# Kernel tuning notes

Measured on AMD Instinct MI355X. Metric: run time of the kernel, lower is better.

## Reference

```python
import jax, jax.numpy as jnp
import numpy as np

N, E, D, H = 50000, 800000, 128, 4
EPS = 1e-5


def setup_inputs() -> dict:
    key = jax.random.key(0)
    ks = jax.random.split(key, 12)
    s_in = 1.0 / np.sqrt(D)
    s_att = 1.0 / np.sqrt(D)
    inp = {
        "x": jax.random.normal(ks[0], (N, D), dtype=jnp.float32),
        "edge_index": jax.random.randint(ks[1], (2, E), 0, N, dtype=jnp.int32),
        # conv1 params: W [D, H*D], att_src/att_dst [H, D], bias [D]
        "W1": jax.random.normal(ks[2], (D, H * D), dtype=jnp.float32) * s_in,
        "as1": jax.random.normal(ks[3], (H, D), dtype=jnp.float32) * s_att,
        "ad1": jax.random.normal(ks[4], (H, D), dtype=jnp.float32) * s_att,
        "b1": jnp.zeros((D,), dtype=jnp.float32),
        "g1": jnp.ones((D,), dtype=jnp.float32),
        "be1": jnp.zeros((D,), dtype=jnp.float32),
        # conv2 params
        "W2": jax.random.normal(ks[5], (D, H * D), dtype=jnp.float32) * s_in,
        "as2": jax.random.normal(ks[6], (H, D), dtype=jnp.float32) * s_att,
        "ad2": jax.random.normal(ks[7], (H, D), dtype=jnp.float32) * s_att,
        "b2": jnp.zeros((D,), dtype=jnp.float32),
        "g2": jnp.ones((D,), dtype=jnp.float32),
        "be2": jnp.zeros((D,), dtype=jnp.float32),
    }
    return inp


def _gat_conv(x, src, dst, W, att_src, att_dst, bias):
    # project: [N, H, C]
    h = (x @ W).reshape(N, H, D)
    a_src = jnp.einsum("nhc,hc->nh", h, att_src)  # [N, H]
    a_dst = jnp.einsum("nhc,hc->nh", h, att_dst)  # [N, H]
    # attention logits per edge, softmax over incoming edges of each dst
    logits = jax.nn.leaky_relu(a_src[src] + a_dst[dst], negative_slope=0.2)  # [Etot, H]
    lmax = jax.ops.segment_max(logits, dst, num_segments=N)  # [N, H]
    p = jnp.exp(logits - lmax[dst])
    denom = jax.ops.segment_sum(p, dst, num_segments=N)  # [N, H]
    alpha = p / denom[dst]  # self-loops guarantee denom > 0
    # weighted scatter-add aggregation
    msg = h[src] * alpha[:, :, None]  # [Etot, H, C]
    out = jax.ops.segment_sum(msg, dst, num_segments=N)  # [N, H, C]
    return out.mean(axis=1) + bias  # concat=False: mean over heads


def _batchnorm_relu(x, gamma, beta):
    mu = x.mean(axis=0)
    var = x.var(axis=0)  # biased, as torch uses for normalization
    xn = (x - mu) * jax.lax.rsqrt(var + EPS)
    return jax.nn.relu(xn * gamma + beta)


def reference(x, edge_index, W1, as1, ad1, b1, g1, be1, W2, as2, ad2, b2, g2, be2):
    # add self loops (GATConv default add_self_loops=True)
    loop = jnp.arange(N, dtype=edge_index.dtype)
    src = jnp.concatenate([edge_index[0], loop])
    dst = jnp.concatenate([edge_index[1], loop])
    x = _batchnorm_relu(_gat_conv(x, src, dst, W1, as1, ad1, b1), g1, be1)
    x = _batchnorm_relu(_gat_conv(x, src, dst, W2, as2, ad2, b2), g2, be2)
    return x
```

## Files before the change

kernel.cpp:

```cpp
#include <hip/hip_runtime.h>
#include <hip/hip_bf16.h>
#include <hip/hip_fp16.h>
#include <math.h>

#define NN 50000
#define NP 50048
#define NE 800000
#define ET (NE + NN)
#define DF 128
#define NH 4
#define HD 512
#define BN_EPS 1e-5f

typedef __hip_bfloat16 bf16;
typedef __attribute__((ext_vector_type(8))) short bf16x8;
typedef __attribute__((ext_vector_type(4))) float f32x4;
typedef __attribute__((ext_vector_type(2))) float f32x2;

__global__ __launch_bounds__(256) void cvt_x_bf16(const float* __restrict__ in, bf16* __restrict__ out) {
    int i = blockIdx.x * 256 + threadIdx.x;
    if (i >= NN * DF / 4) return;
    float4 v = reinterpret_cast<const float4*>(in)[i];
    union { bf16 b[4]; short4 s; } u;
    u.b[0] = __float2bfloat16(v.x); u.b[1] = __float2bfloat16(v.y);
    u.b[2] = __float2bfloat16(v.z); u.b[3] = __float2bfloat16(v.w);
    reinterpret_cast<short4*>(out)[i] = u.s;
}

__global__ __launch_bounds__(256) void make_wsd(const float* __restrict__ W1, const float* __restrict__ as1,
                                                const float* __restrict__ ad1,
                                                const float* __restrict__ W2, const float* __restrict__ as2,
                                                const float* __restrict__ ad2,
                                                float* __restrict__ wsd) {
    int t = blockIdx.x * 256 + threadIdx.x;
    if (t >= 2048) return;
    int layer = t >> 10;
    int o = (t >> 7) & 7;
    int d = t & 127;
    int h = o & 3;
    const float* W  = layer ? W2 : W1;
    const float* av = layer ? (o < 4 ? as2 : ad2) : (o < 4 ? as1 : ad1);
    const float* wrow = W + d * HD + h * DF;
    const float* arow = av + h * DF;
    float sum = 0.f;
    for (int c = 0; c < DF; ++c) sum += wrow[c] * arow[c];
    wsd[layer * 1024 + o * DF + d] = sum;
}

__global__ __launch_bounds__(256) void cvt_bt2(const float* __restrict__ W1, const float* __restrict__ W2,
                                               bf16* __restrict__ B1, bf16* __restrict__ B2) {
    int i = blockIdx.x * 256 + threadIdx.x;
    if (i >= 2 * DF * HD) return;
    int layer = i >> 16;
    int ii = i & 65535;
    int c = ii >> 9, k = ii & 511;
    int h = k >> 7, d = k & 127;
    const float* W = layer ? W2 : W1;
    bf16* B = layer ? B2 : B1;
    B[ii] = __float2bfloat16(0.25f * W[d * HD + h * DF + c]);
}

__global__ __launch_bounds__(256) void xscore(const bf16* __restrict__ X,
                                              const float* __restrict__ wsd,
                                              float* __restrict__ a_src,
                                              float* __restrict__ a_dst,
                                              float* __restrict__ stats) {
    if (blockIdx.x == 0 && threadIdx.x < 64)
        reinterpret_cast<float4*>(stats)[threadIdx.x] = make_float4(0.f, 0.f, 0.f, 0.f);
    __shared__ float w[8][DF];
    reinterpret_cast<float4*>(&w[0][0])[threadIdx.x] = reinterpret_cast<const float4*>(wsd)[threadIdx.x];
    __syncthreads();
    const int n = blockIdx.x * 4 + (threadIdx.x >> 6);
    const int l = threadIdx.x & 63;
    unsigned xv = reinterpret_cast<const unsigned*>(X)[n * 64 + l];
    float x0 = __uint_as_float(xv << 16);
    float x1 = __uint_as_float(xv & 0xffff0000u);
    float v[8];
    #pragma unroll
    for (int o = 0; o < 8; ++o)
        v[o] = x0 * w[o][2 * l] + x1 * w[o][2 * l + 1];
    #pragma unroll
    for (int off = 1; off < 64; off <<= 1) {
        #pragma unroll
        for (int o = 0; o < 8; ++o) v[o] += __shfl_xor(v[o], off);
    }
    if (l == 0) {
        reinterpret_cast<float4*>(a_src)[n] = make_float4(v[0], v[1], v[2], v[3]);
        reinterpret_cast<float4*>(a_dst)[n] = make_float4(v[4], v[5], v[6], v[7]);
    }
}

__global__ __launch_bounds__(256) void count_rank(const int* __restrict__ ei, int* __restrict__ counts,
                                                  int* __restrict__ rank) {
    int e = (blockIdx.x * 256 + threadIdx.x) * 2;
    if (e >= ET) return;
    int d0, d1;
    if (e + 1 < NE) {
        int2 dd = *reinterpret_cast<const int2*>(ei + NE + e);
        d0 = dd.x; d1 = dd.y;
    } else {
        d0 = (e < NE) ? ei[NE + e] : (e - NE);
        d1 = (e + 1 < NE) ? ei[NE + e + 1] : (e + 1 - NE);
    }
    rank[e]     = atomicAdd(&counts[d0 << 4], 1);
    rank[e + 1] = atomicAdd(&counts[d1 << 4], 1);
}

__global__ __launch_bounds__(256) void scan1(const int* __restrict__ counts, int* __restrict__ bsum) {
    __shared__ int sd[256];
    int i = blockIdx.x * 256 + threadIdx.x;
    sd[threadIdx.x] = (i < NN) ? counts[i << 4] : 0;
    __syncthreads();
    for (int s = 128; s > 0; s >>= 1) {
        if (threadIdx.x < s) sd[threadIdx.x] += sd[threadIdx.x + s];
        __syncthreads();
    }
    if (threadIdx.x == 0) bsum[blockIdx.x] = sd[0];
}

__global__ __launch_bounds__(256) void scan2(int* __restrict__ bsum, int nb) {
    __shared__ int sd[256];
    int i = threadIdx.x;
    int v = (i < nb) ? bsum[i] : 0;
    sd[i] = v;
    __syncthreads();
    for (int s = 1; s < 256; s <<= 1) {
        int t = sd[i];
        int u = (i >= s) ? sd[i - s] : 0;
        __syncthreads();
        sd[i] = t + u;
        __syncthreads();
    }
    if (i < nb) bsum[i] = sd[i] - v;
}

__global__ __launch_bounds__(256) void scan3(const int* __restrict__ counts, const int* __restrict__ bsum,
                                             int* __restrict__ row_ptr) {
    __shared__ int sd[256];
    int i = blockIdx.x * 256 + threadIdx.x;
    int v = (i < NN) ? counts[i << 4] : 0;
    sd[threadIdx.x] = v;
    __syncthreads();
    for (int s = 1; s < 256; s <<= 1) {
        int t = sd[threadIdx.x];
        int u = (threadIdx.x >= s) ? sd[threadIdx.x - s] : 0;
        __syncthreads();
        sd[threadIdx.x] = t + u;
        __syncthreads();
    }
    int excl = sd[threadIdx.x] - v + bsum[blockIdx.x];
    if (i < NN) row_ptr[i] = excl;
    if (i == 0) row_ptr[NN] = ET;
}

__global__ __launch_bounds__(256) void fill_scatter(const int* __restrict__ ei, const int* __restrict__ rank,
                                                    const int* __restrict__ row_ptr, int* __restrict__ col) {
    int e = (blockIdx.x * 256 + threadIdx.x) * 2;
    if (e >= ET) return;
    int s0, d0, s1, d1;
    if (e + 1 < NE) {
        int2 ss = *reinterpret_cast<const int2*>(ei + e);
        int2 dd = *reinterpret_cast<const int2*>(ei + NE + e);
        s0 = ss.x; s1 = ss.y; d0 = dd.x; d1 = dd.y;
    } else {
        if (e < NE) { s0 = ei[e]; d0 = ei[NE + e]; } else { s0 = d0 = e - NE; }
        if (e + 1 < NE) { s1 = ei[e + 1]; d1 = ei[NE + e + 1]; } else { s1 = d1 = e + 1 - NE; }
    }
    int2 rk = *reinterpret_cast<const int2*>(rank + e);
    col[row_ptr[d0] + rk.x] = s0;
    col[row_ptr[d1] + rk.y] = s1;
}

#define EDGEF(xu, pa) {                                                              \
    f32x2 xv;                                                                        \
    xv.x = __uint_as_float((xu) << 16);                                              \
    xv.y = __uint_as_float((xu) & 0xffff0000u);                                      \
    acc2[0] += (pa).x * xv;                                                          \
    acc2[1] += (pa).y * xv;                                                          \
    acc2[2] += (pa).z * xv;                                                          \
    acc2[3] += (pa).w * xv; }

#define EDGE(xu, r) {                                                                \
    f32x2 xv;                                                                        \
    xv.x = __uint_as_float((xu) << 16);                                              \
    xv.y = __uint_as_float((xu) & 0xffff0000u);                                      \
    float2 f01 = __half22float2(*reinterpret_cast<const __half2*>(&(r).x));          \
    float2 f23 = __half22float2(*reinterpret_cast<const __half2*>(&(r).y));          \
    acc2[0] += f01.x * xv;                                                           \
    acc2[1] += f01.y * xv;                                                           \
    acc2[2] += f23.x * xv;                                                           \
    acc2[3] += f23.y * xv; }

__global__ __launch_bounds__(256) void agg_fused(const bf16* __restrict__ X,
                                                 const float* __restrict__ a_src,
                                                 const float* __restrict__ a_dst,
                                                 const int* __restrict__ row_ptr,
                                                 const int* __restrict__ col,
                                                 uint4* __restrict__ rec,
                                                 bf16* __restrict__ aggX) {
    __shared__ __align__(16) float4 lalpha[4][64];
    __shared__ unsigned lcol[4][64];
    const int w = threadIdx.x >> 6;
    const int n = blockIdx.x * 4 + w;
    const int l = threadIdx.x & 63;
    const unsigned l4 = (unsigned)l << 2;
    const int start = row_ptr[n], end = row_ptr[n + 1];
    const int deg = end - start;
    const float4 ad4 = reinterpret_cast<const float4*>(a_dst)[n];
    const float4* __restrict__ as4 = reinterpret_cast<const float4*>(a_src);
    const char* __restrict__ Xb = reinterpret_cast<const char*>(X);
    f32x2 acc2[4] = {};
    if (deg <= 64) {
        const int j = start + l;
        int cj = 0;
        float lv[4] = {-1e30f, -1e30f, -1e30f, -1e30f};
        if (j < end) {
            cj = col[j];
            float4 a = as4[cj];
            lv[0] = a.x + ad4.x; lv[1] = a.y + ad4.y; lv[2] = a.z + ad4.z; lv[3] = a.w + ad4.w;
            #pragma unroll
            for (int h = 0; h < 4; ++h) lv[h] = lv[h] > 0.f ? lv[h] : 0.2f * lv[h];
        }
        float m[4], p[4], s[4];
        #pragma unroll
        for (int h = 0; h < 4; ++h) m[h] = lv[h];
        #pragma unroll
        for (int off = 1; off < 64; off <<= 1) {
            #pragma unroll
            for (int h = 0; h < 4; ++h) m[h] = fmaxf(m[h], __shfl_xor(m[h], off));
        }
        #pragma unroll
        for (int h = 0; h < 4; ++h) { p[h] = (j < end) ? __expf(lv[h] - m[h]) : 0.f; s[h] = p[h]; }
        #pragma unroll
        for (int off = 1; off < 64; off <<= 1) {
            #pragma unroll
            for (int h = 0; h < 4; ++h) s[h] += __shfl_xor(s[h], off);
        }
        lalpha[w][l] = make_float4(p[0] / s[0], p[1] / s[1], p[2] / s[2], p[3] / s[3]);
        lcol[w][l] = (unsigned)cj << 8;
        __builtin_amdgcn_wave_barrier();
        for (int i = 0; i < deg; i += 4) {
            float4 pa0 = lalpha[w][i],     pa1 = lalpha[w][i + 1];
            float4 pa2 = lalpha[w][i + 2], pa3 = lalpha[w][i + 3];
            unsigned o0 = lcol[w][i] | l4,     o1 = lcol[w][i + 1] | l4;
            unsigned o2 = lcol[w][i + 2] | l4, o3 = lcol[w][i + 3] | l4;
            unsigned x0 = *reinterpret_cast<const unsigned*>(Xb + o0);
            unsigned x1 = *reinterpret_cast<const unsigned*>(Xb + o1);
            unsigned x2 = *reinterpret_cast<const unsigned*>(Xb + o2);
            unsigned x3 = *reinterpret_cast<const unsigned*>(Xb + o3);
            EDGEF(x0, pa0) EDGEF(x1, pa1) EDGEF(x2, pa2) EDGEF(x3, pa3)
        }
    } else {
        float m[4] = {-1e30f, -1e30f, -1e30f, -1e30f}, s[4] = {0.f, 0.f, 0.f, 0.f};
        for (int base = start; base < end; base += 64) {
            const int j = base + l;
            float lv[4] = {-1e30f, -1e30f, -1e30f, -1e30f};
            if (j < end) {
                float4 a = as4[col[j]];
                lv[0] = a.x + ad4.x; lv[1] = a.y + ad4.y; lv[2] = a.z + ad4.z; lv[3] = a.w + ad4.w;
                #pragma unroll
                for (int h = 0; h < 4; ++h) lv[h] = lv[h] > 0.f ? lv[h] : 0.2f * lv[h];
            }
            float cm[4], cp[4];
            #pragma unroll
            for (int h = 0; h < 4; ++h) cm[h] = lv[h];
            #pragma unroll
            for (int off = 1; off < 64; off <<= 1) {
                #pragma unroll
                for (int h = 0; h < 4; ++h) cm[h] = fmaxf(cm[h], __shfl_xor(cm[h], off));
            }
            #pragma unroll
            for (int h = 0; h < 4; ++h) {
                float nm = fmaxf(m[h], cm[h]);
                cp[h] = (j < end) ? __expf(lv[h] - nm) : 0.f;
                s[h] *= __expf(m[h] - nm);
                m[h] = nm;
            }
            #pragma unroll
            for (int off = 1; off < 64; off <<= 1) {
                #pragma unroll
                for (int h = 0; h < 4; ++h) cp[h] += __shfl_xor(cp[h], off);
            }
            #pragma unroll
            for (int h = 0; h < 4; ++h) s[h] += cp[h];
        }
        for (int base = start; base < end; base += 64) {
            const int j = base + l;
            if (j < end) {
                int cj = col[j];
                float4 a = as4[cj];
                float v0 = a.x + ad4.x, v1 = a.y + ad4.y, v2 = a.z + ad4.z, v3 = a.w + ad4.w;
                v0 = v0 > 0.f ? v0 : 0.2f * v0; v1 = v1 > 0.f ? v1 : 0.2f * v1;
                v2 = v2 > 0.f ? v2 : 0.2f * v2; v3 = v3 > 0.f ? v3 : 0.2f * v3;
                __half2 a01 = __floats2half2_rn(__expf(v0 - m[0]) / s[0], __expf(v1 - m[1]) / s[1]);
                __half2 a23 = __floats2half2_rn(__expf(v2 - m[2]) / s[2], __expf(v3 - m[3]) / s[3]);
                uint4 r;
                r.x = *reinterpret_cast<unsigned*>(&a01);
                r.y = *reinterpret_cast<unsigned*>(&a23);
                r.z = (unsigned)cj;
                r.w = 0;
                rec[j] = r;
            }
        }
        __threadfence_block();
        const unsigned* __restrict__ X4 = reinterpret_cast<const unsigned*>(X);
        int j = start;
        for (; j + 4 <= end; j += 4) {
            uint4 r0 = rec[j], r1 = rec[j + 1], r2 = rec[j + 2], r3 = rec[j + 3];
            unsigned x0 = X4[(size_t)r0.z * 64 + l];
            unsigned x1 = X4[(size_t)r1.z * 64 + l];
            unsigned x2 = X4[(size_t)r2.z * 64 + l];
            unsigned x3 = X4[(size_t)r3.z * 64 + l];
            EDGE(x0, r0) EDGE(x1, r1) EDGE(x2, r2) EDGE(x3, r3)
        }
        for (; j < end; ++j) {
            uint4 r0 = rec[j];
            unsigned x0 = X4[(size_t)r0.z * 64 + l];
            EDGE(x0, r0)
        }
    }
    unsigned* outp = reinterpret_cast<unsigned*>(aggX) + (size_t)n * 256;
    #pragma unroll
    for (int h = 0; h < 4; ++h) {
        union { bf16 b; unsigned short u; } plo, phi;
        plo.b = __float2bfloat16(acc2[h].x);
        phi.b = __float2bfloat16(acc2[h].y);
        outp[h * 64 + l] = (unsigned)plo.u | ((unsigned)phi.u << 16);
    }
}

__global__ __launch_bounds__(256) void gemm_out(const bf16* __restrict__ A,
                                                const bf16* __restrict__ Bt,
                                                const float* __restrict__ bias,
                                                bf16* __restrict__ outb,
                                                float* __restrict__ stats, int M) {
    __shared__ __align__(16) char Bs[65536];
    __shared__ float ssum[128], ssq[128];
    const int tid = threadIdx.x;
    if (tid < 128) { ssum[tid] = 0.f; ssq[tid] = 0.f; }
    const int m0 = blockIdx.x * 64;
    const char* Ab = (const char*)A + (size_t)m0 * 1024;
    const char* Bb = (const char*)Bt;
    auto stageB = [&](int ph) {
        #pragma unroll
        for (int i = 0; i < 16; ++i) {
            int d = (tid + i * 256) * 16;
            int c = d >> 9;
            int kb = d & 511;
            int src = c * 1024 + ph * 512 + (kb ^ ((c & 7) << 4));
            __builtin_amdgcn_global_load_lds(
                (const __attribute__((address_space(1))) void*)(Bb + src),
                (__attribute__((address_space(3))) void*)(Bs + d), 16, 0, 0);
        }
    };
    const int lane = tid & 63;
    const int wave = tid >> 6;
    const int wm = (wave & 1) * 32;
    const int wnb = (wave >> 1) * 64;
    const int lr = lane & 15;
    const int lkb = (lane >> 4) * 16;
    f32x4 acc[2][4] = {};
    const char* arow0 = Ab + (size_t)(wm + lr) * 1024 + lkb;
    const char* arow1 = Ab + (size_t)(wm + 16 + lr) * 1024 + lkb;
    stageB(0);
    #pragma unroll
    for (int ph = 0; ph < 2; ++ph) {
        __syncthreads();
        #pragma unroll 4
        for (int kk = 0; kk < 8; ++kk) {
            int kg = ph * 512 + kk * 64;
            bf16x8 a0 = *(const bf16x8*)(arow0 + kg);
            bf16x8 a1 = *(const bf16x8*)(arow1 + kg);
            int kb = kk * 64 + lkb;
            #pragma unroll
            for (int nf = 0; nf < 4; ++nf) {
                int c = wnb + nf * 16 + lr;
                bf16x8 b = *(const bf16x8*)(Bs + c * 512 + (kb ^ ((c & 7) << 4)));
                acc[0][nf] = __builtin_amdgcn_mfma_f32_16x16x32_bf16(a0, b, acc[0][nf], 0, 0, 0);
                acc[1][nf] = __builtin_amdgcn_mfma_f32_16x16x32_bf16(a1, b, acc[1][nf], 0, 0, 0);
            }
        }
        if (ph == 0) {
            __syncthreads();
            stageB(1);
        }
    }
    const int orow = (lane >> 4) * 4;
    float bcol[4];
    #pragma unroll
    for (int nf = 0; nf < 4; ++nf) bcol[nf] = bias[wnb + nf * 16 + lr];
    #pragma unroll
    for (int nf = 0; nf < 4; ++nf) {
        float cs = 0.f, cq = 0.f;
        int c = wnb + nf * 16 + lr;
        #pragma unroll
        for (int mi = 0; mi < 2; ++mi) {
            #pragma unroll
            for (int r = 0; r < 4; ++r) {
                int gr = m0 + wm + mi * 16 + orow + r;
                if (gr < M) {
                    float v = acc[mi][nf][r] + bcol[nf];
                    outb[(size_t)gr * DF + c] = __float2bfloat16(v);
                    cs += v; cq += v * v;
                }
            }
        }
        atomicAdd(&ssum[c], cs);
        atomicAdd(&ssq[c], cq);
    }
    __syncthreads();
    if (tid < 128) {
        atomicAdd(&stats[tid], ssum[tid]);
        atomicAdd(&stats[128 + tid], ssq[tid]);
    }
}

__device__ __forceinline__ void bn_core(const uint4 v, int c0, const float* stats,
                                        const float* gamma, const float* beta, float* o) {
    float xv[8];
    xv[0] = __uint_as_float(v.x << 16); xv[1] = __uint_as_float(v.x & 0xffff0000u);
    xv[2] = __uint_as_float(v.y << 16); xv[3] = __uint_as_float(v.y & 0xffff0000u);
    xv[4] = __uint_as_float(v.z << 16); xv[5] = __uint_as_float(v.z & 0xffff0000u);
    xv[6] = __uint_as_float(v.w << 16); xv[7] = __uint_as_float(v.w & 0xffff0000u);
    #pragma unroll
    for (int k = 0; k < 8; ++k) {
        int c = c0 + k;
        float mu = stats[c] * (1.f / NN);
        float var = stats[128 + c] * (1.f / NN) - mu * mu;
        o[k] = fmaxf((xv[k] - mu) * rsqrtf(var + BN_EPS) * gamma[c] + beta[c], 0.f);
    }
}

__global__ __launch_bounds__(256) void bn_apply_bf16(const bf16* __restrict__ x, const float* __restrict__ stats,
                                                     const float* __restrict__ gamma, const float* __restrict__ beta,
                                                     bf16* __restrict__ out) {
    int i = blockIdx.x * 256 + threadIdx.x;
    if (i >= NN * DF / 8) return;
    uint4 v = reinterpret_cast<const uint4*>(x)[i];
    float o[8];
    bn_core(v, (i * 8) & 127, stats, gamma, beta, o);
    uint4 w;
    unsigned short* wb = reinterpret_cast<unsigned short*>(&w);
    #pragma unroll
    for (int k = 0; k < 8; ++k) {
        union { bf16 b; unsigned short u; } t;
        t.b = __float2bfloat16(o[k]);
        wb[k] = t.u;
    }
    reinterpret_cast<uint4*>(out)[i] = w;
}

__global__ __launch_bounds__(256) void bn_apply_f32(const bf16* __restrict__ x, const float* __restrict__ stats,
                                                    const float* __restrict__ gamma, const float* __restrict__ beta,
                                                    float* __restrict__ out) {
    int i = blockIdx.x * 256 + threadIdx.x;
    if (i >= NN * DF / 8) return;
    uint4 v = reinterpret_cast<const uint4*>(x)[i];
    float o[8];
    bn_core(v, (i * 8) & 127, stats, gamma, beta, o);
    float4* op = reinterpret_cast<float4*>(out) + (size_t)i * 2;
    op[0] = make_float4(o[0], o[1], o[2], o[3]);
    op[1] = make_float4(o[4], o[5], o[6], o[7]);
}

extern "C" void kernel_launch(void* const* d_in, const int* in_sizes, int n_in,
                              void* d_out, int out_size, void* d_ws, size_t ws_size,
                              hipStream_t stream) {
    (void)in_sizes; (void)n_in; (void)out_size; (void)ws_size;
    const float* x   = (const float*)d_in[0];
    const int*   ei  = (const int*)d_in[1];
    const float* W1  = (const float*)d_in[2];
    const float* as1 = (const float*)d_in[3];
    const float* ad1 = (const float*)d_in[4];
    const float* b1  = (const float*)d_in[5];
    const float* g1  = (const float*)d_in[6];
    const float* be1 = (const float*)d_in[7];
    const float* W2  = (const float*)d_in[8];
    const float* as2 = (const float*)d_in[9];
    const float* ad2 = (const float*)d_in[10];
    const float* b2  = (const float*)d_in[11];
    const float* g2  = (const float*)d_in[12];
    const float* be2 = (const float*)d_in[13];
    float* out = (float*)d_out;

    char* ws = (char*)d_ws;
    size_t off = 0;
    auto alloc = [&](size_t bytes) -> void* {
        void* p = ws + off;
        off += (bytes + 255) & ~(size_t)255;
        return p;
    };
    bf16*   aggX    = (bf16*)alloc((size_t)NP * HD * 2);
    bf16*   xb      = (bf16*)alloc((size_t)NP * DF * 2);
    bf16*   Bt2a    = (bf16*)alloc((size_t)DF * HD * 2);
    bf16*   Bt2b    = (bf16*)alloc((size_t)DF * HD * 2);
    float*  wsd     = (float*)alloc(2 * 1024 * 4);
    float*  a_src   = (float*)alloc((size_t)NN * NH * 4);
    float*  a_dst   = (float*)alloc((size_t)NN * NH * 4);
    int*    row_ptr = (int*)alloc((size_t)(NN + 1) * 4);
    int*    bsum    = (int*)alloc(256 * 4);
    int*    colidx  = (int*)alloc((size_t)ET * 4);
    uint4*  rec     = (uint4*)alloc((size_t)ET * 16);
    bf16*   agg     = (bf16*)alloc((size_t)NN * DF * 2);
    float*  stats   = (float*)alloc(256 * 4);
    int*    counts  = (int*)agg;
    int*    rank    = (int*)((char*)agg + ((size_t)NP << 6));

    const int NB = (NN + 255) / 256;
    const int EB2 = (ET / 2 + 255) / 256;
    const int BNB = (NN * DF / 8 + 255) / 256;

    cvt_x_bf16<<<(NN * DF / 4 + 255) / 256, 256, 0, stream>>>(x, xb);
    make_wsd<<<8, 256, 0, stream>>>(W1, as1, ad1, W2, as2, ad2, wsd);
    cvt_bt2<<<(2 * DF * HD + 255) / 256, 256, 0, stream>>>(W1, W2, Bt2a, Bt2b);
    hipMemsetAsync(counts, 0, (size_t)NP << 6, stream);
    count_rank<<<EB2, 256, 0, stream>>>(ei, counts, rank);
    scan1<<<NB, 256, 0, stream>>>(counts, bsum);
    scan2<<<1, 256, 0, stream>>>(bsum, NB);
    scan3<<<NB, 256, 0, stream>>>(counts, bsum, row_ptr);
    fill_scatter<<<EB2, 256, 0, stream>>>(ei, rank, row_ptr, colidx);

    xscore<<<NN / 4, 256, 0, stream>>>(xb, wsd, a_src, a_dst, stats);
    agg_fused<<<NN / 4, 256, 0, stream>>>(xb, a_src, a_dst, row_ptr, colidx, rec, aggX);
    gemm_out<<<NP / 64, 256, 0, stream>>>(aggX, Bt2a, b1, agg, stats, NN);
    bn_apply_bf16<<<BNB, 256, 0, stream>>>(agg, stats, g1, be1, xb);

    xscore<<<NN / 4, 256, 0, stream>>>(xb, wsd + 1024, a_src, a_dst, stats);
    agg_fused<<<NN / 4, 256, 0, stream>>>(xb, a_src, a_dst, row_ptr, colidx, rec, aggX);
    gemm_out<<<NP / 64, 256, 0, stream>>>(aggX, Bt2b, b2, agg, stats, NN);
    bn_apply_f32<<<BNB, 256, 0, stream>>>(agg, stats, g2, be2, out);
}
```

Baseline: 324.5 us.

## Fuse edge aggregation with output GEMM and replace stats atomics with two-pass reduction

Merges the attention aggregation and the projection GEMM into one kernel. Each block aggregates 16 destination rows into swizzled LDS and then runs MFMA against the weight matrix, so the 51 MB aggX intermediate is never written to or read from global memory. BN statistics now go to per-block scratch and are summed by a separate reduce kernel instead of global atomics. The cost is that each block processes its 4 rows per wave one after another, which lowers parallelism in the gather phase. B is also read straight from global memory or L2 by every block rather than staged in LDS, and an extra kernel launch is added.

```diff
diff --git a/kernel.cpp b/kernel.cpp
--- a/kernel.cpp
+++ b/kernel.cpp
@@ -11,6 +11,7 @@
 #define NH 4
 #define HD 512
 #define BN_EPS 1e-5f
+#define GB (NP / 16)
 
 typedef __hip_bfloat16 bf16;
 typedef __attribute__((ext_vector_type(8))) short bf16x8;
@@ -63,10 +64,7 @@
 __global__ __launch_bounds__(256) void xscore(const bf16* __restrict__ X,
                                               const float* __restrict__ wsd,
                                               float* __restrict__ a_src,
-                                              float* __restrict__ a_dst,
-                                              float* __restrict__ stats) {
-    if (blockIdx.x == 0 && threadIdx.x < 64)
-        reinterpret_cast<float4*>(stats)[threadIdx.x] = make_float4(0.f, 0.f, 0.f, 0.f);
+                                              float* __restrict__ a_dst) {
     __shared__ float w[8][DF];
     reinterpret_cast<float4*>(&w[0][0])[threadIdx.x] = reinterpret_cast<const float4*>(wsd)[threadIdx.x];
     __syncthreads();
@@ -191,228 +189,217 @@
     acc2[2] += f23.x * xv;                                                           \
     acc2[3] += f23.y * xv; }
 
-__global__ __launch_bounds__(256) void agg_fused(const bf16* __restrict__ X,
-                                                 const float* __restrict__ a_src,
-                                                 const float* __restrict__ a_dst,
-                                                 const int* __restrict__ row_ptr,
-                                                 const int* __restrict__ col,
-                                                 uint4* __restrict__ rec,
-                                                 bf16* __restrict__ aggX) {
+__global__ __launch_bounds__(256) void agg_gemm(const bf16* __restrict__ X,
+                                                const float* __restrict__ a_src,
+                                                const float* __restrict__ a_dst,
+                                                const int* __restrict__ row_ptr,
+                                                const int* __restrict__ col,
+                                                uint4* __restrict__ rec,
+                                                const bf16* __restrict__ Bt,
+                                                const float* __restrict__ bias,
+                                                bf16* __restrict__ outb,
+                                                float* __restrict__ scratch, int M) {
+    __shared__ __align__(16) char As[16384];
     __shared__ __align__(16) float4 lalpha[4][64];
     __shared__ unsigned lcol[4][64];
     const int w = threadIdx.x >> 6;
-    const int n = blockIdx.x * 4 + w;
     const int l = threadIdx.x & 63;
     const unsigned l4 = (unsigned)l << 2;
-    const int start = row_ptr[n], end = row_ptr[n + 1];
-    const int deg = end - start;
-    const float4 ad4 = reinterpret_cast<const float4*>(a_dst)[n];
+    const int m0 = blockIdx.x * 16;
     const float4* __restrict__ as4 = reinterpret_cast<const float4*>(a_src);
     const char* __restrict__ Xb = reinterpret_cast<const char*>(X);
-    f32x2 acc2[4] = {};
-    if (deg <= 64) {
-        const int j = start + l;
-        int cj = 0;
-        float lv[4] = {-1e30f, -1e30f, -1e30f, -1e30f};
-        if (j < end) {
-            cj = col[j];
-            float4 a = as4[cj];
-            lv[0] = a.x + ad4.x; lv[1] = a.y + ad4.y; lv[2] = a.z + ad4.z; lv[3] = a.w + ad4.w;
-            #pragma unroll
-            for (int h = 0; h < 4; ++h) lv[h] = lv[h] > 0.f ? lv[h] : 0.2f * lv[h];
-        }
-        float m[4], p[4], s[4];
-        #pragma unroll
-        for (int h = 0; h < 4; ++h) m[h] = lv[h];
-        #pragma unroll
-        for (int off = 1; off < 64; off <<= 1) {
-            #pragma unroll
-            for (int h = 0; h < 4; ++h) m[h] = fmaxf(m[h], __shfl_xor(m[h], off));
+    for (int nn = 0; nn < 4; ++nn) {
+        const int r = w * 4 + nn;
+        const int n = m0 + r;
+        char* rowp = As + r * 1024;
+        const unsigned swz = (unsigned)((r & 7) << 4);
+        f32x2 acc2[4] = {};
+        if (n < NN) {
+            const int start = row_ptr[n], end = row_ptr[n + 1];
+            const int deg = end - start;
+            const float4 ad4 = reinterpret_cast<const float4*>(a_dst)[n];
+            if (deg <= 64) {
+                const int j = start + l;
+                int cj = 0;
+                float lv[4] = {-1e30f, -1e30f, -1e30f, -1e30f};
+                if (j < end) {
+                    cj = col[j];
+                    float4 a = as4[cj];
+                    lv[0] = a.x + ad4.x; lv[1] = a.y + ad4.y; lv[2] = a.z + ad4.z; lv[3] = a.w + ad4.w;
+                    #pragma unroll
+                    for (int h = 0; h < 4; ++h) lv[h] = lv[h] > 0.f ? lv[h] : 0.2f * lv[h];
+                }
+                float m[4], p[4], s[4];
+                #pragma unroll
+                for (int h = 0; h < 4; ++h) m[h] = lv[h];
+                #pragma unroll
+                for (int off = 1; off < 64; off <<= 1) {
+                    #pragma unroll
+                    for (int h = 0; h < 4; ++h) m[h] = fmaxf(m[h], __shfl_xor(m[h], off));
+                }
+                #pragma unroll
+                for (int h = 0; h < 4; ++h) { p[h] = (j < end) ? __expf(lv[h] - m[h]) : 0.f; s[h] = p[h]; }
+                #pragma unroll
+                for (int off = 1; off < 64; off <<= 1) {
+                    #pragma unroll
+                    for (int h = 0; h < 4; ++h) s[h] += __shfl_xor(s[h], off);
+                }
+                lalpha[w][l] = make_float4(p[0] / s[0], p[1] / s[1], p[2] / s[2], p[3] / s[3]);
+                lcol[w][l] = (unsigned)cj << 8;
+                __builtin_amdgcn_wave_barrier();
+                for (int i = 0; i < deg; i += 4) {
+                    float4 pa0 = lalpha[w][i],     pa1 = lalpha[w][i + 1];
+                    float4 pa2 = lalpha[w][i + 2], pa3 = lalpha[w][i + 3];
+                    unsigned o0 = lcol[w][i] | l4,     o1 = lcol[w][i + 1] | l4;
+                    unsigned o2 = lcol[w][i + 2] | l4, o3 = lcol[w][i + 3] | l4;
+                    unsigned x0 = *reinterpret_cast<const unsigned*>(Xb + o0);
+                    unsigned x1 = *reinterpret_cast<const unsigned*>(Xb + o1);
+                    unsigned x2 = *reinterpret_cast<const unsigned*>(Xb + o2);
+                    unsigned x3 = *reinterpret_cast<const unsigned*>(Xb + o3);
+                    EDGEF(x0, pa0) EDGEF(x1, pa1) EDGEF(x2, pa2) EDGEF(x3, pa3)
+                }
+                __builtin_amdgcn_wave_barrier();
+            } else {
+                float m[4] = {-1e30f, -1e30f, -1e30f, -1e30f}, s[4] = {0.f, 0.f, 0.f, 0.f};
+                for (int base = start; base < end; base += 64) {
+                    const int j = base + l;
+                    float lv[4] = {-1e30f, -1e30f, -1e30f, -1e30f};
+                    if (j < end) {
+                        float4 a = as4[col[j]];
+                        lv[0] = a.x + ad4.x; lv[1] = a.y + ad4.y; lv[2] = a.z + ad4.z; lv[3] = a.w + ad4.w;
+                        #pragma unroll
+                        for (int h = 0; h < 4; ++h) lv[h] = lv[h] > 0.f ? lv[h] : 0.2f * lv[h];
+                    }
+                    float cm[4], cp[4];
+                    #pragma unroll
+                    for (int h = 0; h < 4; ++h) cm[h] = lv[h];
+                    #pragma unroll
+                    for (int off = 1; off < 64; off <<= 1) {
+                        #pragma unroll
+                        for (int h = 0; h < 4; ++h) cm[h] = fmaxf(cm[h], __shfl_xor(cm[h], off));
+                    }
+                    #pragma unroll
+                    for (int h = 0; h < 4; ++h) {
+                        float nm = fmaxf(m[h], cm[h]);
+                        cp[h] = (j < end) ? __expf(lv[h] - nm) : 0.f;
+                        s[h] *= __expf(m[h] - nm);
+                        m[h] = nm;
+                    }
+                    #pragma unroll
+                    for (int off = 1; off < 64; off <<= 1) {
+                        #pragma unroll
+                        for (int h = 0; h < 4; ++h) cp[h] += __shfl_xor(cp[h], off);
+                    }
+                    #pragma unroll
+                    for (int h = 0; h < 4; ++h) s[h] += cp[h];
+                }
+                for (int base = start; base < end; base += 64) {
+                    const int j = base + l;
+                    if (j < end) {
+                        int cj = col[j];
+                        float4 a = as4[cj];
+                        float v0 = a.x + ad4.x, v1 = a.y + ad4.y, v2 = a.z + ad4.z, v3 = a.w + ad4.w;
+                        v0 = v0 > 0.f ? v0 : 0.2f * v0; v1 = v1 > 0.f ? v1 : 0.2f * v1;
+                        v2 = v2 > 0.f ? v2 : 0.2f * v2; v3 = v3 > 0.f ? v3 : 0.2f * v3;
+                        __half2 a01 = __floats2half2_rn(__expf(v0 - m[0]) / s[0], __expf(v1 - m[1]) / s[1]);
+                        __half2 a23 = __floats2half2_rn(__expf(v2 - m[2]) / s[2], __expf(v3 - m[3]) / s[3]);
+                        uint4 rr;
+                        rr.x = *reinterpret_cast<unsigned*>(&a01);
+                        rr.y = *reinterpret_cast<unsigned*>(&a23);
+                        rr.z = (unsigned)cj;
+                        rr.w = 0;
+                        rec[j] = rr;
+                    }
+                }
+                __threadfence_block();
+                const unsigned* __restrict__ X4 = reinterpret_cast<const unsigned*>(X);
+                int j = start;
+                for (; j + 4 <= end; j += 4) {
+                    uint4 r0 = rec[j], r1 = rec[j + 1], r2 = rec[j + 2], r3 = rec[j + 3];
+                    unsigned x0 = X4[(size_t)r0.z * 64 + l];
+                    unsigned x1 = X4[(size_t)r1.z * 64 + l];
+                    unsigned x2 = X4[(size_t)r2.z * 64 + l];
+                    unsigned x3 = X4[(size_t)r3.z * 64 + l];
+                    EDGE(x0, r0) EDGE(x1, r1) EDGE(x2, r2) EDGE(x3, r3)
+                }
+                for (; j < end; ++j) {
+                    uint4 r0 = rec[j];
+                    unsigned x0 = X4[(size_t)r0.z * 64 + l];
+                    EDGE(x0, r0)
+                }
+            }
         }
         #pragma unroll
-        for (int h = 0; h < 4; ++h) { p[h] = (j < end) ? __expf(lv[h] - m[h]) : 0.f; s[h] = p[h]; }
+        for (int h = 0; h < 4; ++h) {
+            union { bf16 b; unsigned short u; } plo, phi;
+            plo.b = __float2bfloat16(acc2[h].x);
+            phi.b = __float2bfloat16(acc2[h].y);
+            unsigned u = (unsigned)plo.u | ((unsigned)phi.u << 16);
+            *reinterpret_cast<unsigned*>(rowp + ((h * 256 + l4) ^ swz)) = u;
+        }
+    }
+    __syncthreads();
+    const int lr = l & 15;
+    const int lkb = (l >> 4) * 16;
+    const char* Asr = As + lr * 1024;
+    const unsigned aswz = (unsigned)((lr & 7) << 4);
+    const char* Bb = (const char*)Bt + (size_t)(w * 32) * 1024;
+    f32x4 acc[2] = {};
+    #pragma unroll 4
+    for (int ks = 0; ks < 16; ++ks) {
+        int kg = ks * 64;
+        bf16x8 a  = *(const bf16x8*)(Asr + ((kg + lkb) ^ aswz));
+        bf16x8 b0 = *(const bf16x8*)(Bb + (size_t)lr * 1024 + kg + lkb);
+        bf16x8 b1 = *(const bf16x8*)(Bb + (size_t)(16 + lr) * 1024 + kg + lkb);
+        acc[0] = __builtin_amdgcn_mfma_f32_16x16x32_bf16(a, b0, acc[0], 0, 0, 0);
+        acc[1] = __builtin_amdgcn_mfma_f32_16x16x32_bf16(a, b1, acc[1], 0, 0, 0);
+    }
+    const int orow = (l >> 4) * 4;
+    float cs[2] = {0.f, 0.f}, cq[2] = {0.f, 0.f};
+    #pragma unroll
+    for (int nf = 0; nf < 2; ++nf) {
+        int c = w * 32 + nf * 16 + lr;
+        float bc = bias[c];
         #pragma unroll
-        for (int off = 1; off < 64; off <<= 1) {
-            #pragma unroll
-            for (int h = 0; h < 4; ++h) s[h] += __shfl_xor(s[h], off);
-        }
-        lalpha[w][l] = make_float4(p[0] / s[0], p[1] / s[1], p[2] / s[2], p[3] / s[3]);
-        lcol[w][l] = (unsigned)cj << 8;
-        __builtin_amdgcn_wave_barrier();
-        for (int i = 0; i < deg; i += 4) {
-            float4 pa0 = lalpha[w][i],     pa1 = lalpha[w][i + 1];
-            float4 pa2 = lalpha[w][i + 2], pa3 = lalpha[w][i + 3];
-            unsigned o0 = lcol[w][i] | l4,     o1 = lcol[w][i + 1] | l4;
-            unsigned o2 = lcol[w][i + 2] | l4, o3 = lcol[w][i + 3] | l4;
-            unsigned x0 = *reinterpret_cast<const unsigned*>(Xb + o0);
-            unsigned x1 = *reinterpret_cast<const unsigned*>(Xb + o1);
-            unsigned x2 = *reinterpret_cast<const unsigned*>(Xb + o2);
-            unsigned x3 = *reinterpret_cast<const unsigned*>(Xb + o3);
-            EDGEF(x0, pa0) EDGEF(x1, pa1) EDGEF(x2, pa2) EDGEF(x3, pa3)
-        }
-    } else {
-        float m[4] = {-1e30f, -1e30f, -1e30f, -1e30f}, s[4] = {0.f, 0.f, 0.f, 0.f};
-        for (int base = start; base < end; base += 64) {
-            const int j = base + l;
-            float lv[4] = {-1e30f, -1e30f, -1e30f, -1e30f};
-            if (j < end) {
-                float4 a = as4[col[j]];
-                lv[0] = a.x + ad4.x; lv[1] = a.y + ad4.y; lv[2] = a.z + ad4.z; lv[3] = a.w + ad4.w;
-                #pragma unroll
-                for (int h = 0; h < 4; ++h) lv[h] = lv[h] > 0.f ? lv[h] : 0.2f * lv[h];
-            }
-            float cm[4], cp[4];
-            #pragma unroll
-            for (int h = 0; h < 4; ++h) cm[h] = lv[h];
-            #pragma unroll
-            for (int off = 1; off < 64; off <<= 1) {
-                #pragma unroll
-                for (int h = 0; h < 4; ++h) cm[h] = fmaxf(cm[h], __shfl_xor(cm[h], off));
-            }
-            #pragma unroll
-            for (int h = 0; h < 4; ++h) {
-                float nm = fmaxf(m[h], cm[h]);
-                cp[h] = (j < end) ? __expf(lv[h] - nm) : 0.f;
-                s[h] *= __expf(m[h] - nm);
-                m[h] = nm;
-            }
-            #pragma unroll
-            for (int off = 1; off < 64; off <<= 1) {
-                #pragma unroll
-                for (int h = 0; h < 4; ++h) cp[h] += __shfl_xor(cp[h], off);
-            }
-            #pragma unroll
-            for (int h = 0; h < 4; ++h) s[h] += cp[h];
-        }
-        for (int base = start; base < end; base += 64) {
-            const int j = base + l;
-            if (j < end) {
-                int cj = col[j];
-                float4 a = as4[cj];
-                float v0 = a.x + ad4.x, v1 = a.y + ad4.y, v2 = a.z + ad4.z, v3 = a.w + ad4.w;
-                v0 = v0 > 0.f ? v0 : 0.2f * v0; v1 = v1 > 0.f ? v1 : 0.2f * v1;
-                v2 = v2 > 0.f ? v2 : 0.2f * v2; v3 = v3 > 0.f ? v3 : 0.2f * v3;
-                __half2 a01 = __floats2half2_rn(__expf(v0 - m[0]) / s[0], __expf(v1 - m[1]) / s[1]);
-                __half2 a23 = __floats2half2_rn(__expf(v2 - m[2]) / s[2], __expf(v3 - m[3]) / s[3]);
-                uint4 r;
-                r.x = *reinterpret_cast<unsigned*>(&a01);
-                r.y = *reinterpret_cast<unsigned*>(&a23);
-                r.z = (unsigned)cj;
-                r.w = 0;
-                rec[j] = r;
+        for (int r4 = 0; r4 < 4; ++r4) {
+            int gr = m0 + orow + r4;
+            if (gr < M) {
+                float v = acc[nf][r4] + bc;
+                outb[(size_t)gr * DF + c] = __float2bfloat16(v);
+                cs[nf] += v; cq[nf] += v * v;
             }
         }
-        __threadfence_block();
-        const unsigned* __restrict__ X4 = reinterpret_cast<const unsigned*>(X);
-        int j = start;
-        for (; j + 4 <= end; j += 4) {
-            uint4 r0 = rec[j], r1 = rec[j + 1], r2 = rec[j + 2], r3 = rec[j + 3];
-            unsigned x0 = X4[(size_t)r0.z * 64 + l];
-            unsigned x1 = X4[(size_t)r1.z * 64 + l];
-            unsigned x2 = X4[(size_t)r2.z * 64 + l];
-            unsigned x3 = X4[(size_t)r3.z * 64 + l];
-            EDGE(x0, r0) EDGE(x1, r1) EDGE(x2, r2) EDGE(x3, r3)
+    }
+    #pragma unroll
+    for (int nf = 0; nf < 2; ++nf) {
+        cs[nf] += __shfl_xor(cs[nf], 16);  cq[nf] += __shfl_xor(cq[nf], 16);
+        cs[nf] += __shfl_xor(cs[nf], 32);  cq[nf] += __shfl_xor(cq[nf], 32);
+    }
+    if (l < 16) {
+        float* sp = scratch + (size_t)blockIdx.x * 256;
+        #pragma unroll
+        for (int nf = 0; nf < 2; ++nf) {
+            int c = w * 32 + nf * 16 + l;
+            sp[c] = cs[nf];
+            sp[128 + c] = cq[nf];
         }
-        for (; j < end; ++j) {
-            uint4 r0 = rec[j];
-            unsigned x0 = X4[(size_t)r0.z * 64 + l];
-            EDGE(x0, r0)
-        }
-    }
-    unsigned* outp = reinterpret_cast<unsigned*>(aggX) + (size_t)n * 256;
-    #pragma unroll
-    for (int h = 0; h < 4; ++h) {
-        union { bf16 b; unsigned short u; } plo, phi;
-        plo.b = __float2bfloat16(acc2[h].x);
-        phi.b = __float2bfloat16(acc2[h].y);
-        outp[h * 64 + l] = (unsigned)plo.u | ((unsigned)phi.u << 16);
-    }
-}
-
-__global__ __launch_bounds__(256) void gemm_out(const bf16* __restrict__ A,
-                                                const bf16* __restrict__ Bt,
-                                                const float* __restrict__ bias,
-                                                bf16* __restrict__ outb,
-                                                float* __restrict__ stats, int M) {
-    __shared__ __align__(16) char Bs[65536];
-    __shared__ float ssum[128], ssq[128];
-    const int tid = threadIdx.x;
-    if (tid < 128) { ssum[tid] = 0.f; ssq[tid] = 0.f; }
-    const int m0 = blockIdx.x * 64;
-    const char* Ab = (const char*)A + (size_t)m0 * 1024;
-    const char* Bb = (const char*)Bt;
-    auto stageB = [&](int ph) {
-        #pragma unroll
-        for (int i = 0; i < 16; ++i) {
-            int d = (tid + i * 256) * 16;
-            int c = d >> 9;
-            int kb = d & 511;
-            int src = c * 1024 + ph * 512 + (kb ^ ((c & 7) << 4));
-            __builtin_amdgcn_global_load_lds(
-                (const __attribute__((address_space(1))) void*)(Bb + src),
-                (__attribute__((address_space(3))) void*)(Bs + d), 16, 0, 0);
-        }
-    };
-    const int lane = tid & 63;
-    const int wave = tid >> 6;
-    const int wm = (wave & 1) * 32;
-    const int wnb = (wave >> 1) * 64;
-    const int lr = lane & 15;
-    const int lkb = (lane >> 4) * 16;
-    f32x4 acc[2][4] = {};
-    const char* arow0 = Ab + (size_t)(wm + lr) * 1024 + lkb;
-    const char* arow1 = Ab + (size_t)(wm + 16 + lr) * 1024 + lkb;
-    stageB(0);
-    #pragma unroll
-    for (int ph = 0; ph < 2; ++ph) {
+    }
+}
+
+__global__ __launch_bounds__(256) void stats_reduce(const float* __restrict__ scratch,
+                                                    float* __restrict__ stats) {
+    const int t = blockIdx.x;
+    float s = 0.f;
+    for (int i = threadIdx.x; i < GB; i += 256)
+        s += scratch[(size_t)i * 256 + t];
+    __shared__ float sd[256];
+    sd[threadIdx.x] = s;
+    __syncthreads();
+    for (int o = 128; o > 0; o >>= 1) {
+        if (threadIdx.x < o) sd[threadIdx.x] += sd[threadIdx.x + o];
         __syncthreads();
-        #pragma unroll 4
-        for (int kk = 0; kk < 8; ++kk) {
-            int kg = ph * 512 + kk * 64;
-            bf16x8 a0 = *(const bf16x8*)(arow0 + kg);
-            bf16x8 a1 = *(const bf16x8*)(arow1 + kg);
-            int kb = kk * 64 + lkb;
-            #pragma unroll
-            for (int nf = 0; nf < 4; ++nf) {
-                int c = wnb + nf * 16 + lr;
-                bf16x8 b = *(const bf16x8*)(Bs + c * 512 + (kb ^ ((c & 7) << 4)));
-                acc[0][nf] = __builtin_amdgcn_mfma_f32_16x16x32_bf16(a0, b, acc[0][nf], 0, 0, 0);
-                acc[1][nf] = __builtin_amdgcn_mfma_f32_16x16x32_bf16(a1, b, acc[1][nf], 0, 0, 0);
-            }
-        }
-        if (ph == 0) {
-            __syncthreads();
-            stageB(1);
-        }
-    }
-    const int orow = (lane >> 4) * 4;
-    float bcol[4];
-    #pragma unroll
-    for (int nf = 0; nf < 4; ++nf) bcol[nf] = bias[wnb + nf * 16 + lr];
-    #pragma unroll
-    for (int nf = 0; nf < 4; ++nf) {
-        float cs = 0.f, cq = 0.f;
-        int c = wnb + nf * 16 + lr;
-        #pragma unroll
-        for (int mi = 0; mi < 2; ++mi) {
-            #pragma unroll
-            for (int r = 0; r < 4; ++r) {
-                int gr = m0 + wm + mi * 16 + orow + r;
-                if (gr < M) {
-                    float v = acc[mi][nf][r] + bcol[nf];
-                    outb[(size_t)gr * DF + c] = __float2bfloat16(v);
-                    cs += v; cq += v * v;
-                }
-            }
-        }
-        atomicAdd(&ssum[c], cs);
-        atomicAdd(&ssq[c], cq);
-    }
-    __syncthreads();
-    if (tid < 128) {
-        atomicAdd(&stats[tid], ssum[tid]);
-        atomicAdd(&stats[128 + tid], ssq[tid]);
-    }
+    }
+    if (threadIdx.x == 0) stats[t] = sd[0];
 }
 
 __device__ __forceinline__ void bn_core(const uint4 v, int c0, const float* stats,
@@ -490,7 +477,6 @@
         off += (bytes + 255) & ~(size_t)255;
         return p;
     };
-    bf16*   aggX    = (bf16*)alloc((size_t)NP * HD * 2);
     bf16*   xb      = (bf16*)alloc((size_t)NP * DF * 2);
     bf16*   Bt2a    = (bf16*)alloc((size_t)DF * HD * 2);
     bf16*   Bt2b    = (bf16*)alloc((size_t)DF * HD * 2);
@@ -503,6 +489,7 @@
     uint4*  rec     = (uint4*)alloc((size_t)ET * 16);
     bf16*   agg     = (bf16*)alloc((size_t)NN * DF * 2);
     float*  stats   = (float*)alloc(256 * 4);
+    float*  scratch = (float*)alloc((size_t)GB * 256 * 4);
     int*    counts  = (int*)agg;
     int*    rank    = (int*)((char*)agg + ((size_t)NP << 6));
 
@@ -520,13 +507,13 @@
     scan3<<<NB, 256, 0, stream>>>(counts, bsum, row_ptr);
     fill_scatter<<<EB2, 256, 0, stream>>>(ei, rank, row_ptr, colidx);
 
-    xscore<<<NN / 4, 256, 0, stream>>>(xb, wsd, a_src, a_dst, stats);
-    agg_fused<<<NN / 4, 256, 0, stream>>>(xb, a_src, a_dst, row_ptr, colidx, rec, aggX);
-    gemm_out<<<NP / 64, 256, 0, stream>>>(aggX, Bt2a, b1, agg, stats, NN);
+    xscore<<<NN / 4, 256, 0, stream>>>(xb, wsd, a_src, a_dst);
+    agg_gemm<<<GB, 256, 0, stream>>>(xb, a_src, a_dst, row_ptr, colidx, rec, Bt2a, b1, agg, scratch, NN);
+    stats_reduce<<<256, 256, 0, stream>>>(scratch, stats);
     bn_apply_bf16<<<BNB, 256, 0, stream>>>(agg, stats, g1, be1, xb);
 
-    xscore<<<NN / 4, 256, 0, stream>>>(xb, wsd + 1024, a_src, a_dst, stats);
-    agg_fused<<<NN / 4, 256, 0, stream>>>(xb, a_src, a_dst, row_ptr, colidx, rec, aggX);
-    gemm_out<<<NP / 64, 256, 0, stream>>>(aggX, Bt2b, b2, agg, stats, NN);
+    xscore<<<NN / 4, 256, 0, stream>>>(xb, wsd + 1024, a_src, a_dst);
+    agg_gemm<<<GB, 256, 0, stream>>>(xb, a_src, a_dst, row_ptr, colidx, rec, Bt2b, b2, agg, scratch, NN);
+    stats_reduce<<<256, 256, 0, stream>>>(scratch, stats);
     bn_apply_f32<<<BNB, 256, 0, stream>>>(agg, stats, g2, be2, out);
 }
```

Result: slower. 350.5 us (+8.0%).
